# Performance work log

Hardware: AMD Instinct MI355X
Metric: run time of the kernel (lower is better)

The kernel has to match this reference:

```python
import jax, jax.numpy as jnp
import numpy as np

MAX_DISP = 4          # init kwarg
WIN = 2 * MAX_DISP + 1  # 9 -> 81 displacement offsets
CHUNK = 16            # hardcoded channel chunk size in the torch module


def setup_inputs() -> dict:
    key = jax.random.key(0)
    k1, k2 = jax.random.split(key)
    B, C, H, W = 8, 128, 96, 160
    x1 = jax.random.normal(k1, (B, C, H, W), dtype=jnp.float32)
    x2 = jax.random.normal(k2, (B, C, H, W), dtype=jnp.float32)
    return {"x1": x1, "x2": x2}


def reference(x1, x2):
    B, C, H, W = x2.shape
    pad = MAX_DISP
    # replicate padding == torch F.pad mode='replicate' == jnp 'edge'
    x2p = jnp.pad(x2, ((0, 0), (0, 0), (pad, pad), (pad, pad)), mode="edge")
    # offsets in the same row-major (dy outer, dx inner) order as the torch loops
    dy, dx = jnp.meshgrid(jnp.arange(-pad, pad + 1), jnp.arange(-pad, pad + 1), indexing="ij")
    offsets = jnp.stack([dy.ravel(), dx.ravel()], axis=1)  # [81, 2]
    num_chunks = -(-C // CHUNK)  # ceil(C/16); with C%16==0 chunk-mean == total-sum/num_chunks

    def body(carry, off):
        # shifted window of x2: x2p[:, :, pad+dy : pad+dy+H, pad+dx : pad+dx+W]
        sl = jax.lax.dynamic_slice(x2p, (0, 0, pad + off[0], pad + off[1]), (B, C, H, W))
        return carry, jnp.sum(x1 * sl, axis=1)  # [B, H, W]

    _, corr = jax.lax.scan(body, None, offsets)  # [81, B, H, W]
    corr = jnp.transpose(corr, (1, 0, 2, 3))     # [B, 81, H, W]
    return corr / jnp.asarray(num_chunks, corr.dtype)
```

## Files before the change

### kernel.cpp

```cpp
#include <hip/hip_runtime.h>
#include <cstdint>

#define BB 8
#define CC 128
#define HH 96
#define WW 160
#define HWsz (HH * WW)
#define TH 8
#define TW 32
#define CSTEP 8
#define HALO_H (TH + 8)
#define HALO_W (TW + 8)
#define CH_WORDS (HALO_H * HALO_W)
#define CHUNK_WORDS (CSTEP * CH_WORDS)
#define NWAVES 9
#define NTHREADS (NWAVES * 64)
#define WLOADS (CHUNK_WORDS / 64)
#define NCHUNKS (CC / CSTEP)
#define NBLOCKS (BB * (HH / TH) * (WW / TW))

__device__ __forceinline__ void g2l_dword(const float* g, float* l) {
  __builtin_amdgcn_global_load_lds((const __attribute__((address_space(1))) void*)g,
                                   (__attribute__((address_space(3))) void*)l,
                                   4, 0, 0);
}

extern "C" __global__ void __launch_bounds__(NTHREADS, 4)
corr81_kernel(const float* __restrict__ x1, const float* __restrict__ x2,
              float* __restrict__ out)
{
  __shared__ __align__(16) float lds[CHUNK_WORDS];

  const int tid  = threadIdx.x;
  const int wv   = tid >> 6;
  const int lane = tid & 63;
  const int r    = lane >> 3;
  const int j    = lane & 7;

  const int bid = blockIdx.x;
  const int wt  = bid % (WW / TW);
  const int ht  = (bid / (WW / TW)) % (HH / TH);
  const int b   = bid / ((WW / TW) * (HH / TH));
  const int h0  = ht * TH;
  const int w0  = wt * TW;

  uint32_t soff[9];
#pragma unroll
  for (int i = 0; i < 9; ++i) {
    const int idx = wv + 9 * i;
    const int e   = idx * 64 + lane;
    const int ci  = e / CH_WORDS;
    const int rem = e - ci * CH_WORDS;
    const int hr  = rem / HALO_W;
    const int wh  = rem - hr * HALO_W;
    int gh = h0 + hr - 4; gh = gh < 0 ? 0 : (gh > HH - 1 ? HH - 1 : gh);
    int gw = w0 + wh - 4; gw = gw < 0 ? 0 : (gw > WW - 1 ? WW - 1 : gw);
    soff[i] = (uint32_t)((ci * HH + gh) * WW + gw);
  }

  const float* x2b = x2 + (size_t)b * CC * HWsz;
  const float* x1b = x1 + (size_t)b * CC * HWsz + (size_t)(h0 + r) * WW + (w0 + 4 * j);

  float acc[9][4];
#pragma unroll
  for (int dx = 0; dx < 9; ++dx)
#pragma unroll
    for (int p = 0; p < 4; ++p) acc[dx][p] = 0.f;

  const int rowbase = (r + wv) * HALO_W + 4 * j;

  for (int chunk = 0; chunk < NCHUNKS; ++chunk) {
    const float* x2c = x2b + (size_t)chunk * (CSTEP * HWsz);
#pragma unroll
    for (int i = 0; i < 9; ++i) {
      const int idx = wv + 9 * i;
      if (idx < WLOADS) {
        g2l_dword(x2c + soff[i], &lds[idx * 64]);
      }
    }
    __syncthreads();

#pragma unroll
    for (int ci = 0; ci < CSTEP; ++ci) {
      const float* x1c = x1b + (size_t)(chunk * CSTEP + ci) * HWsz;
      const float4 a4 = *(const float4*)x1c;
      const float av[4] = {a4.x, a4.y, a4.z, a4.w};
      const float4* wr = (const float4*)&lds[ci * CH_WORDS + rowbase];
      const float4 f0 = wr[0];
      const float4 f1 = wr[1];
      const float4 f2 = wr[2];
      const float w12[12] = {f0.x, f0.y, f0.z, f0.w,
                             f1.x, f1.y, f1.z, f1.w,
                             f2.x, f2.y, f2.z, f2.w};
#pragma unroll
      for (int dx = 0; dx < 9; ++dx)
#pragma unroll
        for (int p = 0; p < 4; ++p)
          acc[dx][p] = fmaf(av[p], w12[dx + p], acc[dx][p]);
    }
    __syncthreads();
  }

  float* op = out + (((size_t)b * 81 + (size_t)wv * 9) * HH + (h0 + r)) * WW + (w0 + 4 * j);
#pragma unroll
  for (int dx = 0; dx < 9; ++dx) {
    float4 v;
    v.x = acc[dx][0] * 0.125f;
    v.y = acc[dx][1] * 0.125f;
    v.z = acc[dx][2] * 0.125f;
    v.w = acc[dx][3] * 0.125f;
    *(float4*)(op + (size_t)dx * HWsz) = v;
  }
}

extern "C" void kernel_launch(void* const* d_in, const int* in_sizes, int n_in,
                              void* d_out, int out_size, void* d_ws, size_t ws_size,
                              hipStream_t stream) {
  const float* x1 = (const float*)d_in[0];
  const float* x2 = (const float*)d_in[1];
  float* out = (float*)d_out;
  corr81_kernel<<<dim3(NBLOCKS), dim3(NTHREADS), 0, stream>>>(x1, x2, out);
}
```

Measured before the change: 217.7 us.

## Double-buffer x2 halo in LDS with 16-byte direct global-to-LDS loads

Staging of the x2 halo tile moves from 4-byte to 16-byte global_load_lds transfers, with replicate-edge padding on the left and right image borders now fixed up in registers instead of by clamped per-element addresses. LDS becomes two buffers so the next chunk loads while the current one is computed, which removes one barrier per chunk. The launch-bounds occupancy hint is raised from 4 to 5. The cost is twice the LDS per block, which may limit the number of resident blocks, plus some extra edge-handling logic in the inner loop.

```diff
diff --git a/kernel.cpp b/kernel.cpp
--- a/kernel.cpp
+++ b/kernel.cpp
@@ -15,21 +15,22 @@
 #define CHUNK_WORDS (CSTEP * CH_WORDS)
 #define NWAVES 9
 #define NTHREADS (NWAVES * 64)
-#define WLOADS (CHUNK_WORDS / 64)
 #define NCHUNKS (CC / CSTEP)
 #define NBLOCKS (BB * (HH / TH) * (WW / TW))
+#define NSLOTS (CHUNK_WORDS / 256)
 
-__device__ __forceinline__ void g2l_dword(const float* g, float* l) {
+__device__ __forceinline__ void g2l16(const float* g, float* l) {
   __builtin_amdgcn_global_load_lds((const __attribute__((address_space(1))) void*)g,
                                    (__attribute__((address_space(3))) void*)l,
-                                   4, 0, 0);
+                                   16, 0, 0);
 }
 
-extern "C" __global__ void __launch_bounds__(NTHREADS, 4)
+extern "C" __global__ void __launch_bounds__(NTHREADS, 5)
 corr81_kernel(const float* __restrict__ x1, const float* __restrict__ x2,
               float* __restrict__ out)
 {
-  __shared__ __align__(16) float lds[CHUNK_WORDS];
+  __shared__ __align__(16) float ldsA[CHUNK_WORDS];
+  __shared__ __align__(16) float ldsB[CHUNK_WORDS];
 
   const int tid  = threadIdx.x;
   const int wv   = tid >> 6;
@@ -44,18 +45,23 @@
   const int h0  = ht * TH;
   const int w0  = wt * TW;
 
-  uint32_t soff[9];
+  const int nslot = (wv < 2) ? 3 : 2;
+  int slot_id[3] = {wv, wv + 9, 18 + wv};
+  uint32_t goff[3];
+  uint32_t lbase[3];
 #pragma unroll
-  for (int i = 0; i < 9; ++i) {
-    const int idx = wv + 9 * i;
-    const int e   = idx * 64 + lane;
-    const int ci  = e / CH_WORDS;
-    const int rem = e - ci * CH_WORDS;
+  for (int i = 0; i < 3; ++i) {
+    const int s   = slot_id[i];
+    const int e4  = s * 256 + lane * 4;
+    const int ci  = e4 / CH_WORDS;
+    const int rem = e4 - ci * CH_WORDS;
     const int hr  = rem / HALO_W;
-    const int wh  = rem - hr * HALO_W;
+    const int seg = (rem - hr * HALO_W) >> 2;
     int gh = h0 + hr - 4; gh = gh < 0 ? 0 : (gh > HH - 1 ? HH - 1 : gh);
-    int gw = w0 + wh - 4; gw = gw < 0 ? 0 : (gw > WW - 1 ? WW - 1 : gw);
-    soff[i] = (uint32_t)((ci * HH + gh) * WW + gw);
+    int gw = w0 + seg * 4 - 4;
+    gw = gw < 0 ? 0 : (gw > WW - 4 ? WW - 4 : gw);
+    goff[i]  = (uint32_t)(ci * HWsz + gh * WW + gw);
+    lbase[i] = (uint32_t)(s * 256);
   }
 
   const float* x2b = x2 + (size_t)b * CC * HWsz;
@@ -68,36 +74,51 @@
     for (int p = 0; p < 4; ++p) acc[dx][p] = 0.f;
 
   const int rowbase = (r + wv) * HALO_W + 4 * j;
+  const bool ledge = (w0 == 0);
+  const bool redge = (w0 == WW - TW);
 
-  for (int chunk = 0; chunk < NCHUNKS; ++chunk) {
-    const float* x2c = x2b + (size_t)chunk * (CSTEP * HWsz);
+  auto stage = [&](int chunk, float* buf) {
+    const float* src = x2b + (size_t)chunk * (CSTEP * HWsz);
 #pragma unroll
-    for (int i = 0; i < 9; ++i) {
-      const int idx = wv + 9 * i;
-      if (idx < WLOADS) {
-        g2l_dword(x2c + soff[i], &lds[idx * 64]);
-      }
-    }
-    __syncthreads();
+    for (int i = 0; i < 3; ++i)
+      if (i < nslot)
+        g2l16(src + goff[i], buf + lbase[i]);
+  };
 
+  auto compute = [&](int chunk, const float* buf) {
 #pragma unroll
     for (int ci = 0; ci < CSTEP; ++ci) {
-      const float* x1c = x1b + (size_t)(chunk * CSTEP + ci) * HWsz;
-      const float4 a4 = *(const float4*)x1c;
+      const float4 a4 = *(const float4*)(x1b + (size_t)(chunk * CSTEP + ci) * HWsz);
       const float av[4] = {a4.x, a4.y, a4.z, a4.w};
-      const float4* wr = (const float4*)&lds[ci * CH_WORDS + rowbase];
-      const float4 f0 = wr[0];
-      const float4 f1 = wr[1];
-      const float4 f2 = wr[2];
-      const float w12[12] = {f0.x, f0.y, f0.z, f0.w,
-                             f1.x, f1.y, f1.z, f1.w,
-                             f2.x, f2.y, f2.z, f2.w};
+      const float* wp = buf + ci * CH_WORDS + rowbase;
+      const float4 f0 = *(const float4*)(wp);
+      const float4 f1 = *(const float4*)(wp + 4);
+      const float4 f2 = *(const float4*)(wp + 8);
+      float w12[12] = {f0.x, f0.y, f0.z, f0.w,
+                       f1.x, f1.y, f1.z, f1.w,
+                       f2.x, f2.y, f2.z, f2.w};
+      if (ledge) {
+        if (j == 0) { w12[0] = w12[4]; w12[1] = w12[4]; w12[2] = w12[4]; w12[3] = w12[4]; }
+      }
+      if (redge) {
+        if (j == 7) { w12[8] = w12[7]; w12[9] = w12[7]; w12[10] = w12[7]; w12[11] = w12[7]; }
+      }
 #pragma unroll
       for (int dx = 0; dx < 9; ++dx)
 #pragma unroll
         for (int p = 0; p < 4; ++p)
           acc[dx][p] = fmaf(av[p], w12[dx + p], acc[dx][p]);
     }
+  };
+
+  stage(0, ldsA);
+  __syncthreads();
+  for (int chunk = 0; chunk < NCHUNKS; chunk += 2) {
+    stage(chunk + 1, ldsB);
+    compute(chunk, ldsA);
+    __syncthreads();
+    if (chunk + 2 < NCHUNKS) stage(chunk + 2, ldsA);
+    compute(chunk + 1, ldsB);
     __syncthreads();
   }
 
```

Result: slower. 538.3 us (+147.3%).

## Drop LDS staging; load x2 rows directly from global, split dy across blocks

Applied to the files above, without the earlier changes.

Replaces the LDS halo tile, which was filled with global_load_lds and guarded by two barriers per channel chunk, with direct float4 global loads of the shifted x2 rows. Replicate padding is now handled by clamping rows and column offsets, with fixups for edge lanes. The nine dy rows are split over three times as many blocks of three waves each, so each block covers three dy values and runs no barriers. The cost is redundant global and L2 reads of x1 and x2 across blocks and waves, plus more blocks to schedule.

```diff
diff --git a/kernel.cpp b/kernel.cpp
--- a/kernel.cpp
+++ b/kernel.cpp
@@ -8,29 +8,15 @@
 #define HWsz (HH * WW)
 #define TH 8
 #define TW 32
-#define CSTEP 8
-#define HALO_H (TH + 8)
-#define HALO_W (TW + 8)
-#define CH_WORDS (HALO_H * HALO_W)
-#define CHUNK_WORDS (CSTEP * CH_WORDS)
-#define NWAVES 9
+#define NWAVES 3
 #define NTHREADS (NWAVES * 64)
-#define WLOADS (CHUNK_WORDS / 64)
-#define NCHUNKS (CC / CSTEP)
-#define NBLOCKS (BB * (HH / TH) * (WW / TW))
-
-__device__ __forceinline__ void g2l_dword(const float* g, float* l) {
-  __builtin_amdgcn_global_load_lds((const __attribute__((address_space(1))) void*)g,
-                                   (__attribute__((address_space(3))) void*)l,
-                                   4, 0, 0);
-}
+#define NTILES (BB * (HH / TH) * (WW / TW))
+#define NBLOCKS (3 * NTILES)
 
 extern "C" __global__ void __launch_bounds__(NTHREADS, 4)
 corr81_kernel(const float* __restrict__ x1, const float* __restrict__ x2,
               float* __restrict__ out)
 {
-  __shared__ __align__(16) float lds[CHUNK_WORDS];
-
   const int tid  = threadIdx.x;
   const int wv   = tid >> 6;
   const int lane = tid & 63;
@@ -40,26 +26,27 @@
   const int bid = blockIdx.x;
   const int wt  = bid % (WW / TW);
   const int ht  = (bid / (WW / TW)) % (HH / TH);
-  const int b   = bid / ((WW / TW) * (HH / TH));
+  const int b   = (bid / ((WW / TW) * (HH / TH))) % BB;
+  const int g   = bid / NTILES;
   const int h0  = ht * TH;
   const int w0  = wt * TW;
 
-  uint32_t soff[9];
-#pragma unroll
-  for (int i = 0; i < 9; ++i) {
-    const int idx = wv + 9 * i;
-    const int e   = idx * 64 + lane;
-    const int ci  = e / CH_WORDS;
-    const int rem = e - ci * CH_WORDS;
-    const int hr  = rem / HALO_W;
-    const int wh  = rem - hr * HALO_W;
-    int gh = h0 + hr - 4; gh = gh < 0 ? 0 : (gh > HH - 1 ? HH - 1 : gh);
-    int gw = w0 + wh - 4; gw = gw < 0 ? 0 : (gw > WW - 1 ? WW - 1 : gw);
-    soff[i] = (uint32_t)((ci * HH + gh) * WW + gw);
-  }
+  const int dyi = 3 * g + wv;
+  const int dy  = dyi - 4;
+  const int orow = h0 + r;
+  int srow = orow + dy;
+  srow = srow < 0 ? 0 : (srow > HH - 1 ? HH - 1 : srow);
 
-  const float* x2b = x2 + (size_t)b * CC * HWsz;
-  const float* x1b = x1 + (size_t)b * CC * HWsz + (size_t)(h0 + r) * WW + (w0 + 4 * j);
+  const int c1 = w0 + 4 * j;
+  int s0 = c1 - 4; s0 = s0 < 0 ? 0 : s0;
+  const int s1 = c1;
+  int s2 = c1 + 4; s2 = s2 > WW - 4 ? WW - 4 : s2;
+
+  const bool ledge = (w0 == 0);
+  const bool redge = (w0 == WW - TW);
+
+  const float* x1p = x1 + (size_t)b * CC * HWsz + (size_t)orow * WW + c1;
+  const float* x2p = x2 + (size_t)b * CC * HWsz + (size_t)srow * WW;
 
   float acc[9][4];
 #pragma unroll
@@ -67,41 +54,31 @@
 #pragma unroll
     for (int p = 0; p < 4; ++p) acc[dx][p] = 0.f;
 
-  const int rowbase = (r + wv) * HALO_W + 4 * j;
-
-  for (int chunk = 0; chunk < NCHUNKS; ++chunk) {
-    const float* x2c = x2b + (size_t)chunk * (CSTEP * HWsz);
+#pragma unroll 2
+  for (int c = 0; c < CC; ++c) {
+    const size_t coff = (size_t)c * HWsz;
+    const float4 a4 = *(const float4*)(x1p + coff);
+    const float4 f0 = *(const float4*)(x2p + coff + s0);
+    const float4 f1 = *(const float4*)(x2p + coff + s1);
+    const float4 f2 = *(const float4*)(x2p + coff + s2);
+    float w12[12] = {f0.x, f0.y, f0.z, f0.w,
+                     f1.x, f1.y, f1.z, f1.w,
+                     f2.x, f2.y, f2.z, f2.w};
+    if (ledge) {
+      if (j == 0) { w12[0] = w12[4]; w12[1] = w12[4]; w12[2] = w12[4]; w12[3] = w12[4]; }
+    }
+    if (redge) {
+      if (j == 7) { w12[8] = w12[7]; w12[9] = w12[7]; w12[10] = w12[7]; w12[11] = w12[7]; }
+    }
+    const float av[4] = {a4.x, a4.y, a4.z, a4.w};
 #pragma unroll
-    for (int i = 0; i < 9; ++i) {
-      const int idx = wv + 9 * i;
-      if (idx < WLOADS) {
-        g2l_dword(x2c + soff[i], &lds[idx * 64]);
-      }
-    }
-    __syncthreads();
-
+    for (int dx = 0; dx < 9; ++dx)
 #pragma unroll
-    for (int ci = 0; ci < CSTEP; ++ci) {
-      const float* x1c = x1b + (size_t)(chunk * CSTEP + ci) * HWsz;
-      const float4 a4 = *(const float4*)x1c;
-      const float av[4] = {a4.x, a4.y, a4.z, a4.w};
-      const float4* wr = (const float4*)&lds[ci * CH_WORDS + rowbase];
-      const float4 f0 = wr[0];
-      const float4 f1 = wr[1];
-      const float4 f2 = wr[2];
-      const float w12[12] = {f0.x, f0.y, f0.z, f0.w,
-                             f1.x, f1.y, f1.z, f1.w,
-                             f2.x, f2.y, f2.z, f2.w};
-#pragma unroll
-      for (int dx = 0; dx < 9; ++dx)
-#pragma unroll
-        for (int p = 0; p < 4; ++p)
-          acc[dx][p] = fmaf(av[p], w12[dx + p], acc[dx][p]);
-    }
-    __syncthreads();
+      for (int p = 0; p < 4; ++p)
+        acc[dx][p] = fmaf(av[p], w12[dx + p], acc[dx][p]);
   }
 
-  float* op = out + (((size_t)b * 81 + (size_t)wv * 9) * HH + (h0 + r)) * WW + (w0 + 4 * j);
+  float* op = out + (((size_t)b * 81 + (size_t)dyi * 9) * HH + orow) * WW + c1;
 #pragma unroll
   for (int dx = 0; dx < 9; ++dx) {
     float4 v;
```

Result: slower. 245.5 us (+12.8%).
